# Optimization experiments

Measured on AMD Instinct MI355X. Metric: run time of the kernel, lower is better.

The kernel has to match this reference:

```python
import jax, jax.numpy as jnp
import numpy as np

B, C, H, W = 2, 64, 128, 128
K, SCALE, NUM_RES = 3, 2, 2
KK = K * K


def conv(x, w, b, pad=0):
    y = jax.lax.conv_general_dilated(x, w, (1, 1), [(pad, pad), (pad, pad)],
                                     dimension_numbers=('NCHW', 'OIHW', 'NCHW'))
    return y + b[None, :, None, None]


def unfold_dilated(x, k, d):
    # mimics nn.Unfold(kernel_size=k, dilation=d, padding=(k//2)*d) -> (b, c, k*k, h, w)
    pad = (k // 2) * d
    b, c, h, w = x.shape
    xp = jnp.pad(x, ((0, 0), (0, 0), (pad, pad), (pad, pad)))
    slices = [xp[:, :, i * d:i * d + h, j * d:j * d + w]
              for i in range(k) for j in range(k)]
    return jnp.stack(slices, axis=2)


def setup_inputs() -> dict:
    key = jax.random.key(0)
    ks = jax.random.split(key, 32)
    def p(k, shape, s=0.05):
        return jax.random.normal(k, shape, dtype=jnp.float32) * s
    H2, W2 = H * SCALE, W * SCALE
    return {
        'depth':  p(ks[0], (B, C, H2, W2), 1.0),
        'guide':  p(ks[1], (B, C, H2, W2), 1.0),
        'inputs': p(ks[2], (B, C, H, W), 1.0),
        # depth_kernel branch: 1x1 C->C (ReLU), 1x1 C->k^2
        'dk_w1': p(ks[3], (C, C, 1, 1)), 'dk_b1': jnp.zeros((C,), jnp.float32),
        'dk_w2': p(ks[4], (KK, C, 1, 1)), 'dk_b2': jnp.zeros((KK,), jnp.float32),
        # guide_kernel branch
        'gk_w1': p(ks[5], (C, C, 1, 1)), 'gk_b1': jnp.zeros((C,), jnp.float32),
        'gk_w2': p(ks[6], (KK, C, 1, 1)), 'gk_b2': jnp.zeros((KK,), jnp.float32),
        # weight_net: 3x3 2C->C (ReLU), 3x3 C->C (ReLU, TUnet stand-in), 3x3 C->1
        'wn_w1': p(ks[7], (C, 2 * C, 3, 3)), 'wn_b1': jnp.zeros((C,), jnp.float32),
        'wn_w2': p(ks[8], (C, C, 3, 3)), 'wn_b2': jnp.zeros((C,), jnp.float32),
        'wn_w3': p(ks[9], (1, C, 3, 3)), 'wn_b3': jnp.zeros((1,), jnp.float32),
        # residual blocks on inputs: NUM_RES x (conv3x3-ReLU-conv3x3 + skip)
        'rb_w': p(ks[10], (NUM_RES, 2, C, C, 3, 3)),
        'rb_b': jnp.zeros((NUM_RES, 2, C), jnp.float32),
        'aff_scale': 0.5 * KK * jnp.ones((1,), jnp.float32),
    }


def reference(depth, guide, inputs,
              dk_w1, dk_b1, dk_w2, dk_b2,
              gk_w1, gk_b1, gk_w2, gk_b2,
              wn_w1, wn_b1, wn_w2, wn_b2, wn_w3, wn_b3,
              rb_w, rb_b, aff_scale):
    # weight map
    wm = jax.nn.relu(conv(jnp.concatenate([depth, guide], axis=1), wn_w1, wn_b1, 1))
    wm = jax.nn.relu(conv(wm, wn_w2, wn_b2, 1))
    weight_map = conv(wm, wn_w3, wn_b3, 1)                       # (b,1,h_,w_)
    # per-pixel kernels
    dk = conv(jax.nn.relu(conv(depth, dk_w1, dk_b1)), dk_w2, dk_b2)
    gk = conv(jax.nn.relu(conv(guide, gk_w1, gk_b1)), gk_w2, gk_b2)
    dk = jax.nn.softmax(dk, axis=1)
    gk = jax.nn.softmax(gk, axis=1)
    fuse = weight_map * dk + (1.0 - weight_map) * gk
    fuse = jnp.tanh(fuse) / (aff_scale + 1e-8)
    ksum = jnp.maximum(jnp.sum(jnp.abs(fuse), axis=1, keepdims=True) + 1e-4, 1.0)
    fuse = fuse / ksum                                            # (b,k^2,h_,w_)
    # residual conv stack on low-res inputs
    x = inputs
    for i in range(NUM_RES):
        r = jax.nn.relu(conv(x, rb_w[i, 0], rb_b[i, 0], 1))
        r = conv(r, rb_w[i, 1], rb_b[i, 1], 1)
        x = x + r
    b, c, h, w = x.shape
    up = jax.image.resize(x, (b, c, h * SCALE, w * SCALE), method='bilinear')
    unf = unfold_dilated(up, K, SCALE)                            # (b,c,k^2,h_,w_)
    out = jnp.einsum('bkhw,bckhw->bchw', fuse, unf)
    return out
```

## Files before the change

### kernel.cpp

```cpp
#include <hip/hip_runtime.h>
#include <hip/hip_bf16.h>
#include <math.h>

#define HW2 (256*256)
#define HW1 (128*128)

typedef __attribute__((ext_vector_type(8))) short short8;
typedef __attribute__((ext_vector_type(4))) float floatx4;

__device__ __forceinline__ float b2f(ushort u) {
    union { unsigned int i; float f; } v; v.i = ((unsigned int)u) << 16; return v.f;
}
__device__ __forceinline__ ushort f2b(float f) {
    __hip_bfloat16 h = __float2bfloat16(f); return *(ushort*)&h;
}

__global__ __launch_bounds__(256)
void repack_w_bf16(const float* __restrict__ w, ushort* __restrict__ wt, int Cin) {
    int idx = blockIdx.x * 256 + threadIdx.x;
    int total = 64 * Cin * 9;
    if (idx >= total) return;
    int o   = idx / (Cin * 9);
    int rem = idx - o * (Cin * 9);
    int ci  = rem / 9;
    int t   = rem - ci * 9;
    int cc = ci >> 5, cl = ci & 31;
    wt[(((size_t)cc * 9 + t) * 64 + o) * 32 + cl] = f2b(w[idx]);
}

__global__ __launch_bounds__(256)
void repack_w64_batched(const float* __restrict__ wn_w2, const float* __restrict__ rb_w,
                        ushort* __restrict__ wt_wn2, ushort* __restrict__ wt_rb) {
    int idx = blockIdx.x * 256 + threadIdx.x;
    if (idx >= 36864) return;
    int set = blockIdx.y;
    const float* w = (set == 0) ? wn_w2 : rb_w + (size_t)(set - 1) * 36864;
    ushort* wt     = (set == 0) ? wt_wn2 : wt_rb + (size_t)(set - 1) * 36864;
    int o   = idx / 576;
    int rem = idx - o * 576;
    int ci  = rem / 9;
    int t   = rem - ci * 9;
    int cc = ci >> 5, cl = ci & 31;
    wt[(((size_t)cc * 9 + t) * 64 + o) * 32 + cl] = f2b(w[idx]);
}

__global__ __launch_bounds__(256)
void repack_1x1(const float* __restrict__ dk_w1, const float* __restrict__ gk_w1,
                const float* __restrict__ dk_w2, const float* __restrict__ gk_w2,
                ushort* __restrict__ w1d, ushort* __restrict__ w1g,
                ushort* __restrict__ w2d, ushort* __restrict__ w2g) {
    int idx = blockIdx.x * 256 + threadIdx.x;
    int set = blockIdx.y;
    if (set < 2) {
        if (idx >= 4096) return;
        const float* s = set == 0 ? dk_w1 : gk_w1;
        ushort* d = set == 0 ? w1d : w1g;
        d[idx] = f2b(s[idx]);
    } else {
        if (idx >= 1024) return;
        const float* s = set == 2 ? dk_w2 : gk_w2;
        ushort* d = set == 2 ? w2d : w2g;
        int row = idx >> 6;
        d[idx] = (row < 9) ? f2b(s[idx]) : (ushort)0;
    }
}

__global__ __launch_bounds__(256)
void to_chunked(const float* __restrict__ in, ushort* __restrict__ outc,
                int H, int W, int Cchunks) {
    int P = W + 2, Q = H + 2;
    int plane_px = P * Q;
    int idx = blockIdx.x * 256 + threadIdx.x;
    if (idx >= plane_px) return;
    int py = idx / P, px = idx - py * P;
    int bc = blockIdx.y;
    int b = bc / Cchunks, cc = bc - b * Cchunks;
    ushort* dst = outc + ((size_t)bc * plane_px + idx) * 32;
    if (py == 0 || py == Q - 1 || px == 0 || px == P - 1) {
        for (int c = 0; c < 32; ++c) dst[c] = 0;
        return;
    }
    int y = py - 1, x = px - 1;
    const float* src = in + ((size_t)b * (Cchunks * 32) + cc * 32) * H * W
                          + (size_t)y * W + x;
    for (int c = 0; c < 32; ++c)
        dst[c] = f2b(src[(size_t)c * H * W]);
}

__global__ __launch_bounds__(256)
void to_chunked_hi(const float* __restrict__ depth, const float* __restrict__ guide,
                   ushort* __restrict__ outc) {
    const int P = 258;
    int plane_px = P * P;
    int idx = blockIdx.x * 256 + threadIdx.x;
    if (idx >= plane_px) return;
    int py = idx / P, px = idx - py * P;
    int pl = blockIdx.y;
    const float* srcb = (pl < 4) ? depth : guide;
    int bc = pl & 3;
    int b = bc >> 1, cc = bc & 1;
    ushort* dst = outc + ((size_t)pl * plane_px + idx) * 32;
    if (py == 0 || py == P - 1 || px == 0 || px == P - 1) {
        for (int c = 0; c < 32; ++c) dst[c] = 0;
        return;
    }
    int y = py - 1, x = px - 1;
    const float* src = srcb + ((size_t)b * 64 + cc * 32) * HW2 + (size_t)y * 256 + x;
    for (int c = 0; c < 32; ++c)
        dst[c] = f2b(src[(size_t)c * HW2]);
}

__global__ __launch_bounds__(256)
void zero_border(ushort* __restrict__ buf, int H, int W, int nplanes) {
    int P = W + 2, Q = H + 2;
    int nb = 2 * P + 2 * H;
    int idx = blockIdx.x * 256 + threadIdx.x;
    if (idx >= nb * nplanes) return;
    int pl = idx / nb, r = idx - pl * nb;
    int py, px;
    if (r < P)          { py = 0;     px = r; }
    else if (r < 2 * P) { py = Q - 1; px = r - P; }
    else { int k = r - 2 * P; py = 1 + (k >> 1); px = (k & 1) ? P - 1 : 0; }
    ushort* dst = buf + ((size_t)pl * P * Q + (size_t)py * P + px) * 32;
    for (int c = 0; c < 32; ++c) dst[c] = 0;
}

template<int NCHUNK, bool RELU, bool HAS_SKIP, bool CONCAT2>
__global__ __launch_bounds__(256)
void conv3x3_reg(const ushort* __restrict__ inA, const ushort* __restrict__ inB,
                 const ushort* __restrict__ wt, const float* __restrict__ bias,
                 const ushort* __restrict__ skip, ushort* __restrict__ outc,
                 int H, int W) {
    const int P = W + 2;
    const size_t plane = (size_t)P * (H + 2) * 32;
    int tid = threadIdx.x;
    int wv = tid >> 6, lane = tid & 63, ml = lane & 15, q = lane >> 4;
    int x0 = blockIdx.x * 16;
    int rowsPerBlock = (blockDim.x >> 6) * 4;
    int yb = blockIdx.y * rowsPerBlock + wv * 4;
    int b = blockIdx.z;

    floatx4 acc[4][4];
#pragma unroll
    for (int r = 0; r < 4; ++r)
#pragma unroll
        for (int n = 0; n < 4; ++n) acc[r][n] = (floatx4){0.f, 0.f, 0.f, 0.f};

    for (int cc = 0; cc < NCHUNK; ++cc) {
        const ushort* base;
        if (CONCAT2) {
            constexpr int HC = NCHUNK / 2;
            if (cc < HC) base = inA + ((size_t)(b * HC + cc)) * plane;
            else         base = inB + ((size_t)(b * HC + cc - HC)) * plane;
        } else {
            base = inA + ((size_t)(b * NCHUNK + cc)) * plane;
        }
        const ushort* wb = wt + (size_t)cc * 18432;
#pragma unroll
        for (int t = 0; t < 9; ++t) {
            int dy = t / 3, dx = t - 3 * dy;
            short8 afr[4], bfr[4];
#pragma unroll
            for (int r = 0; r < 4; ++r)
                afr[r] = *(const short8*)&base[((size_t)(yb + r + dy) * P
                                               + (x0 + ml + dx)) * 32 + q * 8];
#pragma unroll
            for (int n = 0; n < 4; ++n)
                bfr[n] = *(const short8*)&wb[(size_t)(t * 64 + n * 16 + ml) * 32 + q * 8];
#pragma unroll
            for (int r = 0; r < 4; ++r)
#pragma unroll
                for (int n = 0; n < 4; ++n)
                    acc[r][n] = __builtin_amdgcn_mfma_f32_16x16x32_bf16(
                        afr[r], bfr[n], acc[r][n], 0, 0, 0);
        }
    }

#pragma unroll
    for (int r = 0; r < 4; ++r) {
        int y = yb + r;
#pragma unroll
        for (int n = 0; n < 4; ++n) {
            int ch = n * 16 + ml;
            int occ = ch >> 5, ocl = ch & 31;
            float bs = bias[ch];
            size_t pbase = ((size_t)(b * 2 + occ)) * plane + ((size_t)(y + 1) * P) * 32 + ocl;
#pragma unroll
            for (int e = 0; e < 4; ++e) {
                int x = x0 + q * 4 + e;
                float v = acc[r][n][e] + bs;
                if (RELU) v = fmaxf(v, 0.f);
                if (HAS_SKIP)
                    v += b2f(skip[((size_t)(b * 2 + occ)) * plane
                                  + ((size_t)(y + 1) * P + (x + 1)) * 32 + ocl]);
                outc[pbase + (size_t)(x + 1) * 32] = f2b(v);
            }
        }
    }
}

__global__ __launch_bounds__(256)
void conv3x3_1out_c(const ushort* __restrict__ inc, const float* __restrict__ w,
                    const float* __restrict__ bias, float* __restrict__ out) {
    __shared__ float wl[576];
    int tid = threadIdx.x;
    for (int i = tid; i < 576; i += 256) wl[i] = w[i];
    __syncthreads();

    int x = blockIdx.x * 16 + (tid & 15);
    int y = blockIdx.y * 16 + (tid >> 4);
    int b = blockIdx.z;
    const int P = 258;
    const size_t plane = (size_t)P * 258 * 32;

    float acc = bias[0];
    for (int cc = 0; cc < 2; ++cc) {
        const ushort* base = inc + ((size_t)(b * 2 + cc)) * plane;
#pragma unroll
        for (int t = 0; t < 9; ++t) {
            int dy = t / 3, dx = t - 3 * dy;
            const ushort* p = base + ((size_t)(y + dy) * P + (x + dx)) * 32;
            for (int c = 0; c < 32; ++c)
                acc = fmaf(wl[(cc * 32 + c) * 9 + t], b2f(p[c]), acc);
        }
    }
    out[(size_t)b * HW2 + y * 256 + x] = acc;
}

__global__ __launch_bounds__(256)
void kernels_fuse_mfma(const ushort* __restrict__ depth_c, const ushort* __restrict__ guide_c,
                       const float* __restrict__ wmap,
                       const ushort* __restrict__ w1d, const float* __restrict__ b1d,
                       const ushort* __restrict__ w2d, const float* __restrict__ b2d,
                       const ushort* __restrict__ w1g, const float* __restrict__ b1g,
                       const ushort* __restrict__ w2g, const float* __restrict__ b2g,
                       const float* __restrict__ aff, float* __restrict__ fuse_out) {
    __shared__ __align__(16) ushort hid[2][4][16 * 72];

    int tid = threadIdx.x;
    int wv = tid >> 6, lane = tid & 63, ml = lane & 15, q = lane >> 4;
    int p0 = blockIdx.x * 64 + wv * 16;
    int b = p0 >> 16, rem0 = p0 & 65535;
    const size_t plane = (size_t)258 * 258 * 32;

    int rem = rem0 + ml;
    int y = rem >> 8, x = rem & 255;
    size_t poff = ((size_t)(y + 1) * 258 + (x + 1)) * 32;

    float sm[2][4];

    for (int br = 0; br < 2; ++br) {
        const ushort* src = br ? guide_c : depth_c;
        const ushort* w1  = br ? w1g : w1d;
        const float*  b1  = br ? b1g : b1d;
        const ushort* w2  = br ? w2g : w2d;
        const float*  b2  = br ? b2g : b2d;
        ushort* h = hid[br][wv];

        short8 afr[2];
#pragma unroll
        for (int kc = 0; kc < 2; ++kc)
            afr[kc] = *(const short8*)&src[(size_t)(b * 2 + kc) * plane + poff + q * 8];

        floatx4 acc[4];
#pragma unroll
        for (int nt = 0; nt < 4; ++nt) acc[nt] = (floatx4){0.f, 0.f, 0.f, 0.f};
#pragma unroll
        for (int nt = 0; nt < 4; ++nt)
#pragma unroll
            for (int kc = 0; kc < 2; ++kc) {
                short8 bfr = *(const short8*)&w1[(size_t)((nt * 16 + ml) * 64 + kc * 32 + q * 8)];
                acc[nt] = __builtin_amdgcn_mfma_f32_16x16x32_bf16(afr[kc], bfr, acc[nt], 0, 0, 0);
            }

#pragma unroll
        for (int nt = 0; nt < 4; ++nt) {
            float bs = b1[nt * 16 + ml];
#pragma unroll
            for (int e = 0; e < 4; ++e) {
                float v = acc[nt][e] + bs;
                v = fmaxf(v, 0.f);
                h[(q * 4 + e) * 72 + nt * 16 + ml] = f2b(v);
            }
        }
        __syncthreads();

        floatx4 d2 = (floatx4){0.f, 0.f, 0.f, 0.f};
#pragma unroll
        for (int kc = 0; kc < 2; ++kc) {
            short8 a2 = *(const short8*)&w2[(size_t)(ml * 64 + kc * 32 + q * 8)];
            short8 hf = *(const short8*)&h[ml * 72 + kc * 32 + q * 8];
            d2 = __builtin_amdgcn_mfma_f32_16x16x32_bf16(a2, hf, d2, 0, 0, 0);
        }

        float lg[4];
#pragma unroll
        for (int e = 0; e < 4; ++e) {
            int j = q * 4 + e;
            lg[e] = (j < 9) ? (d2[e] + b2[j]) : -1e30f;
        }
        float m = fmaxf(fmaxf(lg[0], lg[1]), fmaxf(lg[2], lg[3]));
        m = fmaxf(m, __shfl_xor(m, 16));
        m = fmaxf(m, __shfl_xor(m, 32));
        float s = 0.f;
#pragma unroll
        for (int e = 0; e < 4; ++e) { lg[e] = __expf(lg[e] - m); s += lg[e]; }
        s += __shfl_xor(s, 16);
        s += __shfl_xor(s, 32);
        float inv = 1.f / s;
#pragma unroll
        for (int e = 0; e < 4; ++e) sm[br][e] = lg[e] * inv;
    }

    float wm = wmap[p0 + ml];
    float inv_av = 1.f / (aff[0] + 1e-8f);
    float f[4];
    float s = 0.f;
#pragma unroll
    for (int e = 0; e < 4; ++e) {
        float v = wm * sm[0][e] + (1.f - wm) * sm[1][e];
        v = tanhf(v) * inv_av;
        f[e] = v;
        s += fabsf(v);
    }
    s += __shfl_xor(s, 16);
    s += __shfl_xor(s, 32);
    float ksum = s + 1e-4f;
    if (ksum < 1.f) ksum = 1.f;
    float invk = 1.f / ksum;
#pragma unroll
    for (int e = 0; e < 4; ++e) {
        int j = q * 4 + e;
        if (j < 9)
            fuse_out[((size_t)b * 9 + j) * HW2 + rem0 + ml] = f[e] * invk;
    }
}

__global__ __launch_bounds__(256)
void upsample2x_c(const ushort* __restrict__ inc, ushort* __restrict__ outc) {
    int idx = blockIdx.x * 256 + threadIdx.x;
    if (idx >= 260 * 260) return;
    int py = idx / 260, px = idx - py * 260;
    int pl = blockIdx.y;
    ushort* dst = outc + ((size_t)pl * 260 * 260 + idx) * 32;
    if (py < 2 || py >= 258 || px < 2 || px >= 258) {
        for (int c = 0; c < 32; ++c) dst[c] = 0;
        return;
    }
    int y = py - 2, x = px - 2;

    int ylo, yhi; float wylo, wyhi;
    if (y & 1) { ylo = y >> 1; yhi = ylo + 1; if (yhi > 127) yhi = 127; wylo = 0.75f; wyhi = 0.25f; }
    else       { yhi = y >> 1; ylo = yhi - 1; if (ylo < 0)   ylo = 0;   wyhi = 0.75f; wylo = 0.25f; }
    int xlo, xhi; float wxlo, wxhi;
    if (x & 1) { xlo = x >> 1; xhi = xlo + 1; if (xhi > 127) xhi = 127; wxlo = 0.75f; wxhi = 0.25f; }
    else       { xhi = x >> 1; xlo = xhi - 1; if (xlo < 0)   xlo = 0;   wxhi = 0.75f; wxlo = 0.25f; }

    const ushort* base = inc + (size_t)pl * 130 * 130 * 32;
    const ushort* p00 = base + ((size_t)(ylo + 1) * 130 + (xlo + 1)) * 32;
    const ushort* p01 = base + ((size_t)(ylo + 1) * 130 + (xhi + 1)) * 32;
    const ushort* p10 = base + ((size_t)(yhi + 1) * 130 + (xlo + 1)) * 32;
    const ushort* p11 = base + ((size_t)(yhi + 1) * 130 + (xhi + 1)) * 32;
#pragma unroll
    for (int c = 0; c < 32; ++c) {
        float v = wylo * (wxlo * b2f(p00[c]) + wxhi * b2f(p01[c]))
                + wyhi * (wxlo * b2f(p10[c]) + wxhi * b2f(p11[c]));
        dst[c] = f2b(v);
    }
}

__global__ __launch_bounds__(256)
void fuse_apply_c(const float* __restrict__ fuse, const ushort* __restrict__ up,
                  float* __restrict__ out) {
    int p = blockIdx.x * 256 + threadIdx.x;
    int pl = blockIdx.y;
    int b = pl >> 1, cc = pl & 1;
    int y = p >> 8, x = p & 255;

    const float* f = fuse + (size_t)b * 9 * HW2 + p;
    const ushort* ub = up + (size_t)pl * 260 * 260 * 32;

    float acc[32];
#pragma unroll
    for (int c = 0; c < 32; ++c) acc[c] = 0.f;
#pragma unroll
    for (int t = 0; t < 9; ++t) {
        int dy = (t / 3 - 1) * 2, dx = (t % 3 - 1) * 2;
        float fv = f[(size_t)t * HW2];
        const ushort* u = ub + ((size_t)(y + 2 + dy) * 260 + (x + 2 + dx)) * 32;
#pragma unroll
        for (int c = 0; c < 32; ++c) acc[c] = fmaf(fv, b2f(u[c]), acc[c]);
    }
    float* ob = out + ((size_t)(b * 64 + cc * 32)) * HW2 + p;
#pragma unroll
    for (int c = 0; c < 32; ++c) ob[(size_t)c * HW2] = acc[c];
}

extern "C" void kernel_launch(void* const* d_in, const int* in_sizes, int n_in,
                              void* d_out, int out_size, void* d_ws, size_t ws_size,
                              hipStream_t stream) {
    const float* depth  = (const float*)d_in[0];
    const float* guide  = (const float*)d_in[1];
    const float* inputs = (const float*)d_in[2];
    const float* dk_w1  = (const float*)d_in[3];
    const float* dk_b1  = (const float*)d_in[4];
    const float* dk_w2  = (const float*)d_in[5];
    const float* dk_b2  = (const float*)d_in[6];
    const float* gk_w1  = (const float*)d_in[7];
    const float* gk_b1  = (const float*)d_in[8];
    const float* gk_w2  = (const float*)d_in[9];
    const float* gk_b2  = (const float*)d_in[10];
    const float* wn_w1  = (const float*)d_in[11];
    const float* wn_b1  = (const float*)d_in[12];
    const float* wn_w2  = (const float*)d_in[13];
    const float* wn_b2  = (const float*)d_in[14];
    const float* wn_w3  = (const float*)d_in[15];
    const float* wn_b3  = (const float*)d_in[16];
    const float* rb_w   = (const float*)d_in[17];
    const float* rb_b   = (const float*)d_in[18];
    const float* aff    = (const float*)d_in[19];
    float* out = (float*)d_out;

    float* ws = (float*)d_ws;
    size_t off = 0;
    const size_t CH256 = 4260096;
    const size_t CH128 = 1081600;
    ushort* depth_c = (ushort*)(ws + off); off += CH256;
    ushort* guide_c = (ushort*)(ws + off); off += CH256;
    ushort* bufA    = (ushort*)(ws + off); off += CH256;
    ushort* bufB    = (ushort*)(ws + off); off += CH256;
    ushort* up      = bufA;
    ushort* inp_c   = (ushort*)(ws + off); off += CH128;
    ushort* r0      = (ushort*)(ws + off); off += CH128;
    ushort* r1      = (ushort*)(ws + off); off += CH128;
    ushort* r2      = (ushort*)(ws + off); off += CH128;
    float* fuse     = ws + off; off += 1179648;
    float* wmap     = ws + off; off += 131072;
    ushort* wt_wn1  = (ushort*)(ws + off); off += 36864;
    ushort* wt_wn2  = (ushort*)(ws + off); off += 18432;
    ushort* wt_rb   = (ushort*)(ws + off); off += 73728;
    ushort* w1d_b   = (ushort*)(ws + off); off += 2048;
    ushort* w1g_b   = (ushort*)(ws + off); off += 2048;
    ushort* w2d_b   = (ushort*)(ws + off); off += 512;
    ushort* w2g_b   = (ushort*)(ws + off); off += 512;

    repack_w_bf16<<<288, 256, 0, stream>>>(wn_w1, wt_wn1, 128);
    repack_w64_batched<<<dim3(144, 5), 256, 0, stream>>>(wn_w2, rb_w, wt_wn2, wt_rb);
    repack_1x1<<<dim3(16, 4), 256, 0, stream>>>(dk_w1, gk_w1, dk_w2, gk_w2,
                                                w1d_b, w1g_b, w2d_b, w2g_b);

    to_chunked_hi<<<dim3(261, 8), 256, 0, stream>>>(depth, guide, depth_c);
    to_chunked<<<dim3(67, 4), 256, 0, stream>>>(inputs, inp_c, 128, 128, 2);

    zero_border<<<17, 256, 0, stream>>>(bufA, 256, 256, 8);
    zero_border<<<9,  256, 0, stream>>>(r0,   128, 128, 8);

    conv3x3_reg<4, true, false, true ><<<dim3(16, 16, 2), 256, 0, stream>>>(
        depth_c, guide_c, wt_wn1, wn_b1, nullptr, bufA, 256, 256);
    conv3x3_reg<2, true, false, false><<<dim3(16, 16, 2), 256, 0, stream>>>(
        bufA, nullptr, wt_wn2, wn_b2, nullptr, bufB, 256, 256);
    conv3x3_1out_c<<<dim3(16, 16, 2), 256, 0, stream>>>(bufB, wn_w3, wn_b3, wmap);

    kernels_fuse_mfma<<<2048, 256, 0, stream>>>(depth_c, guide_c, wmap,
                                                w1d_b, dk_b1, w2d_b, dk_b2,
                                                w1g_b, gk_b1, w2g_b, gk_b2,
                                                aff, fuse);

    conv3x3_reg<2, true,  false, false><<<dim3(8, 16, 2), 128, 0, stream>>>(
        inp_c, nullptr, wt_rb + 0 * 36864, rb_b + 0 * 64, nullptr, r0, 128, 128);
    conv3x3_reg<2, false, true,  false><<<dim3(8, 16, 2), 128, 0, stream>>>(
        r0, nullptr, wt_rb + 1 * 36864, rb_b + 1 * 64, inp_c, r1, 128, 128);
    conv3x3_reg<2, true,  false, false><<<dim3(8, 16, 2), 128, 0, stream>>>(
        r1, nullptr, wt_rb + 2 * 36864, rb_b + 2 * 64, nullptr, r0, 128, 128);
    conv3x3_reg<2, false, true,  false><<<dim3(8, 16, 2), 128, 0, stream>>>(
        r0, nullptr, wt_rb + 3 * 36864, rb_b + 3 * 64, r1, r2, 128, 128);

    upsample2x_c<<<dim3(265, 4), 256, 0, stream>>>(r2, up);
    fuse_apply_c<<<dim3(256, 4), 256, 0, stream>>>(fuse, up, out);
}
```

Measured before the change: 350.2 us.

## Fuse bilinear upsample into apply and weight-map conv into kernel-fuse

The separate bilinear upsample kernel is removed. The 3x3 dilated taps are now folded with the bilinear weights into a 4x4 coefficient grid, so the final apply kernel reads the low-res residual output directly instead of a materialized upsampled buffer. The single-output 3x3 weight-map conv moves into the per-pixel kernel-fusion kernel, which drops the wmap buffer. The three weight-repack launches are merged into one, the two border-zero launches are merged into one, and the residual convs now run 2 rows per wave with 256-thread blocks. This trades several launches and a large intermediate write and read for more gather loads and register pressure in the fused kernels.

```diff
diff --git a/kernel.cpp b/kernel.cpp
--- a/kernel.cpp
+++ b/kernel.cpp
@@ -16,52 +16,34 @@
 }
 
 __global__ __launch_bounds__(256)
-void repack_w_bf16(const float* __restrict__ w, ushort* __restrict__ wt, int Cin) {
-    int idx = blockIdx.x * 256 + threadIdx.x;
-    int total = 64 * Cin * 9;
-    if (idx >= total) return;
-    int o   = idx / (Cin * 9);
-    int rem = idx - o * (Cin * 9);
-    int ci  = rem / 9;
-    int t   = rem - ci * 9;
-    int cc = ci >> 5, cl = ci & 31;
-    wt[(((size_t)cc * 9 + t) * 64 + o) * 32 + cl] = f2b(w[idx]);
-}
-
-__global__ __launch_bounds__(256)
-void repack_w64_batched(const float* __restrict__ wn_w2, const float* __restrict__ rb_w,
-                        ushort* __restrict__ wt_wn2, ushort* __restrict__ wt_rb) {
-    int idx = blockIdx.x * 256 + threadIdx.x;
-    if (idx >= 36864) return;
-    int set = blockIdx.y;
-    const float* w = (set == 0) ? wn_w2 : rb_w + (size_t)(set - 1) * 36864;
-    ushort* wt     = (set == 0) ? wt_wn2 : wt_rb + (size_t)(set - 1) * 36864;
-    int o   = idx / 576;
-    int rem = idx - o * 576;
-    int ci  = rem / 9;
-    int t   = rem - ci * 9;
-    int cc = ci >> 5, cl = ci & 31;
-    wt[(((size_t)cc * 9 + t) * 64 + o) * 32 + cl] = f2b(w[idx]);
-}
-
-__global__ __launch_bounds__(256)
-void repack_1x1(const float* __restrict__ dk_w1, const float* __restrict__ gk_w1,
+void repack_all(const float* __restrict__ wn_w1, const float* __restrict__ wn_w2,
+                const float* __restrict__ rb_w,
+                const float* __restrict__ dk_w1, const float* __restrict__ gk_w1,
                 const float* __restrict__ dk_w2, const float* __restrict__ gk_w2,
+                ushort* __restrict__ wt_wn1, ushort* __restrict__ wt_wn2,
+                ushort* __restrict__ wt_rb,
                 ushort* __restrict__ w1d, ushort* __restrict__ w1g,
                 ushort* __restrict__ w2d, ushort* __restrict__ w2g) {
     int idx = blockIdx.x * 256 + threadIdx.x;
-    int set = blockIdx.y;
-    if (set < 2) {
-        if (idx >= 4096) return;
-        const float* s = set == 0 ? dk_w1 : gk_w1;
-        ushort* d = set == 0 ? w1d : w1g;
-        d[idx] = f2b(s[idx]);
+    int role = blockIdx.y;
+    if (role == 0) {
+        if (idx >= 73728) return;
+        int o = idx / 1152; int rem = idx - o * 1152;
+        int ci = rem / 9;   int t = rem - ci * 9;
+        wt_wn1[(((size_t)(ci >> 5) * 9 + t) * 64 + o) * 32 + (ci & 31)] = f2b(wn_w1[idx]);
+    } else if (role <= 5) {
+        if (idx >= 36864) return;
+        const float* w = (role == 1) ? wn_w2 : rb_w + (size_t)(role - 2) * 36864;
+        ushort* wt     = (role == 1) ? wt_wn2 : wt_rb + (size_t)(role - 2) * 36864;
+        int o = idx / 576; int rem = idx - o * 576;
+        int ci = rem / 9;  int t = rem - ci * 9;
+        wt[(((size_t)(ci >> 5) * 9 + t) * 64 + o) * 32 + (ci & 31)] = f2b(w[idx]);
     } else {
-        if (idx >= 1024) return;
-        const float* s = set == 2 ? dk_w2 : gk_w2;
-        ushort* d = set == 2 ? w2d : w2g;
-        int row = idx >> 6;
-        d[idx] = (row < 9) ? f2b(s[idx]) : (ushort)0;
+        if (idx >= 10240) return;
+        if (idx < 4096)      w1d[idx] = f2b(dk_w1[idx]);
+        else if (idx < 8192) w1g[idx - 4096] = f2b(gk_w1[idx - 4096]);
+        else if (idx < 9216) { int i = idx - 8192; w2d[i] = (i >> 6) < 9 ? f2b(dk_w2[i]) : (ushort)0; }
+        else                 { int i = idx - 9216; w2g[i] = (i >> 6) < 9 ? f2b(gk_w2[i]) : (ushort)0; }
     }
 }
 
@@ -111,11 +93,14 @@
 }
 
 __global__ __launch_bounds__(256)
-void zero_border(ushort* __restrict__ buf, int H, int W, int nplanes) {
-    int P = W + 2, Q = H + 2;
+void zero_border2(ushort* __restrict__ buf256, ushort* __restrict__ buf128) {
+    int region = blockIdx.y;
+    int H = region ? 128 : 256;
+    int P = H + 2, Q = H + 2;
+    ushort* buf = region ? buf128 : buf256;
     int nb = 2 * P + 2 * H;
     int idx = blockIdx.x * 256 + threadIdx.x;
-    if (idx >= nb * nplanes) return;
+    if (idx >= nb * 8) return;
     int pl = idx / nb, r = idx - pl * nb;
     int py, px;
     if (r < P)          { py = 0;     px = r; }
@@ -125,7 +110,7 @@
     for (int c = 0; c < 32; ++c) dst[c] = 0;
 }
 
-template<int NCHUNK, bool RELU, bool HAS_SKIP, bool CONCAT2>
+template<int NCHUNK, int ROWS, bool RELU, bool HAS_SKIP, bool CONCAT2>
 __global__ __launch_bounds__(256)
 void conv3x3_reg(const ushort* __restrict__ inA, const ushort* __restrict__ inB,
                  const ushort* __restrict__ wt, const float* __restrict__ bias,
@@ -136,13 +121,13 @@
     int tid = threadIdx.x;
     int wv = tid >> 6, lane = tid & 63, ml = lane & 15, q = lane >> 4;
     int x0 = blockIdx.x * 16;
-    int rowsPerBlock = (blockDim.x >> 6) * 4;
-    int yb = blockIdx.y * rowsPerBlock + wv * 4;
+    int rowsPerBlock = (blockDim.x >> 6) * ROWS;
+    int yb = blockIdx.y * rowsPerBlock + wv * ROWS;
     int b = blockIdx.z;
 
-    floatx4 acc[4][4];
-#pragma unroll
-    for (int r = 0; r < 4; ++r)
+    floatx4 acc[ROWS][4];
+#pragma unroll
+    for (int r = 0; r < ROWS; ++r)
 #pragma unroll
         for (int n = 0; n < 4; ++n) acc[r][n] = (floatx4){0.f, 0.f, 0.f, 0.f};
 
@@ -159,16 +144,16 @@
 #pragma unroll
         for (int t = 0; t < 9; ++t) {
             int dy = t / 3, dx = t - 3 * dy;
-            short8 afr[4], bfr[4];
-#pragma unroll
-            for (int r = 0; r < 4; ++r)
+            short8 afr[ROWS], bfr[4];
+#pragma unroll
+            for (int r = 0; r < ROWS; ++r)
                 afr[r] = *(const short8*)&base[((size_t)(yb + r + dy) * P
                                                + (x0 + ml + dx)) * 32 + q * 8];
 #pragma unroll
             for (int n = 0; n < 4; ++n)
                 bfr[n] = *(const short8*)&wb[(size_t)(t * 64 + n * 16 + ml) * 32 + q * 8];
 #pragma unroll
-            for (int r = 0; r < 4; ++r)
+            for (int r = 0; r < ROWS; ++r)
 #pragma unroll
                 for (int n = 0; n < 4; ++n)
                     acc[r][n] = __builtin_amdgcn_mfma_f32_16x16x32_bf16(
@@ -177,7 +162,7 @@
     }
 
 #pragma unroll
-    for (int r = 0; r < 4; ++r) {
+    for (int r = 0; r < ROWS; ++r) {
         int y = yb + r;
 #pragma unroll
         for (int n = 0; n < 4; ++n) {
@@ -200,44 +185,21 @@
 }
 
 __global__ __launch_bounds__(256)
-void conv3x3_1out_c(const ushort* __restrict__ inc, const float* __restrict__ w,
-                    const float* __restrict__ bias, float* __restrict__ out) {
-    __shared__ float wl[576];
-    int tid = threadIdx.x;
-    for (int i = tid; i < 576; i += 256) wl[i] = w[i];
-    __syncthreads();
-
-    int x = blockIdx.x * 16 + (tid & 15);
-    int y = blockIdx.y * 16 + (tid >> 4);
-    int b = blockIdx.z;
-    const int P = 258;
-    const size_t plane = (size_t)P * 258 * 32;
-
-    float acc = bias[0];
-    for (int cc = 0; cc < 2; ++cc) {
-        const ushort* base = inc + ((size_t)(b * 2 + cc)) * plane;
-#pragma unroll
-        for (int t = 0; t < 9; ++t) {
-            int dy = t / 3, dx = t - 3 * dy;
-            const ushort* p = base + ((size_t)(y + dy) * P + (x + dx)) * 32;
-            for (int c = 0; c < 32; ++c)
-                acc = fmaf(wl[(cc * 32 + c) * 9 + t], b2f(p[c]), acc);
-        }
-    }
-    out[(size_t)b * HW2 + y * 256 + x] = acc;
-}
-
-__global__ __launch_bounds__(256)
 void kernels_fuse_mfma(const ushort* __restrict__ depth_c, const ushort* __restrict__ guide_c,
-                       const float* __restrict__ wmap,
+                       const ushort* __restrict__ bufB,
+                       const float* __restrict__ wn_w3, const float* __restrict__ wn_b3,
                        const ushort* __restrict__ w1d, const float* __restrict__ b1d,
                        const ushort* __restrict__ w2d, const float* __restrict__ b2d,
                        const ushort* __restrict__ w1g, const float* __restrict__ b1g,
                        const ushort* __restrict__ w2g, const float* __restrict__ b2g,
                        const float* __restrict__ aff, float* __restrict__ fuse_out) {
     __shared__ __align__(16) ushort hid[2][4][16 * 72];
+    __shared__ float wl[576];
 
     int tid = threadIdx.x;
+    for (int i = tid; i < 576; i += 256) wl[i] = wn_w3[i];
+    __syncthreads();
+
     int wv = tid >> 6, lane = tid & 63, ml = lane & 15, q = lane >> 4;
     int p0 = blockIdx.x * 64 + wv * 16;
     int b = p0 >> 16, rem0 = p0 & 65535;
@@ -247,8 +209,19 @@
     int y = rem >> 8, x = rem & 255;
     size_t poff = ((size_t)(y + 1) * 258 + (x + 1)) * 32;
 
+    float wm = wn_b3[0];
+    for (int cc = 0; cc < 2; ++cc) {
+        const ushort* basep = bufB + (size_t)(b * 2 + cc) * plane;
+#pragma unroll
+        for (int t = 0; t < 9; ++t) {
+            int dy = t / 3, dx = t - 3 * dy;
+            const ushort* pp = basep + ((size_t)(y + dy) * 258 + (x + dx)) * 32;
+            for (int c = 0; c < 32; ++c)
+                wm = fmaf(wl[(cc * 32 + c) * 9 + t], b2f(pp[c]), wm);
+        }
+    }
+
     float sm[2][4];
-
     for (int br = 0; br < 2; ++br) {
         const ushort* src = br ? guide_c : depth_c;
         const ushort* w1  = br ? w1g : w1d;
@@ -283,7 +256,6 @@
                 h[(q * 4 + e) * 72 + nt * 16 + ml] = f2b(v);
             }
         }
-        __syncthreads();
 
         floatx4 d2 = (floatx4){0.f, 0.f, 0.f, 0.f};
 #pragma unroll
@@ -312,7 +284,6 @@
         for (int e = 0; e < 4; ++e) sm[br][e] = lg[e] * inv;
     }
 
-    float wm = wmap[p0 + ml];
     float inv_av = 1.f / (aff[0] + 1e-8f);
     float f[4];
     float s = 0.f;
@@ -337,59 +308,57 @@
 }
 
 __global__ __launch_bounds__(256)
-void upsample2x_c(const ushort* __restrict__ inc, ushort* __restrict__ outc) {
-    int idx = blockIdx.x * 256 + threadIdx.x;
-    if (idx >= 260 * 260) return;
-    int py = idx / 260, px = idx - py * 260;
-    int pl = blockIdx.y;
-    ushort* dst = outc + ((size_t)pl * 260 * 260 + idx) * 32;
-    if (py < 2 || py >= 258 || px < 2 || px >= 258) {
-        for (int c = 0; c < 32; ++c) dst[c] = 0;
-        return;
-    }
-    int y = py - 2, x = px - 2;
-
-    int ylo, yhi; float wylo, wyhi;
-    if (y & 1) { ylo = y >> 1; yhi = ylo + 1; if (yhi > 127) yhi = 127; wylo = 0.75f; wyhi = 0.25f; }
-    else       { yhi = y >> 1; ylo = yhi - 1; if (ylo < 0)   ylo = 0;   wyhi = 0.75f; wylo = 0.25f; }
-    int xlo, xhi; float wxlo, wxhi;
-    if (x & 1) { xlo = x >> 1; xhi = xlo + 1; if (xhi > 127) xhi = 127; wxlo = 0.75f; wxhi = 0.25f; }
-    else       { xhi = x >> 1; xlo = xhi - 1; if (xlo < 0)   xlo = 0;   wxhi = 0.75f; wxlo = 0.25f; }
-
-    const ushort* base = inc + (size_t)pl * 130 * 130 * 32;
-    const ushort* p00 = base + ((size_t)(ylo + 1) * 130 + (xlo + 1)) * 32;
-    const ushort* p01 = base + ((size_t)(ylo + 1) * 130 + (xhi + 1)) * 32;
-    const ushort* p10 = base + ((size_t)(yhi + 1) * 130 + (xlo + 1)) * 32;
-    const ushort* p11 = base + ((size_t)(yhi + 1) * 130 + (xhi + 1)) * 32;
-#pragma unroll
-    for (int c = 0; c < 32; ++c) {
-        float v = wylo * (wxlo * b2f(p00[c]) + wxhi * b2f(p01[c]))
-                + wyhi * (wxlo * b2f(p10[c]) + wxhi * b2f(p11[c]));
-        dst[c] = f2b(v);
-    }
-}
-
-__global__ __launch_bounds__(256)
-void fuse_apply_c(const float* __restrict__ fuse, const ushort* __restrict__ up,
-                  float* __restrict__ out) {
+void fuse_apply_up(const float* __restrict__ fuse, const ushort* __restrict__ r2c,
+                   float* __restrict__ out) {
     int p = blockIdx.x * 256 + threadIdx.x;
     int pl = blockIdx.y;
     int b = pl >> 1, cc = pl & 1;
     int y = p >> 8, x = p & 255;
 
+    int my = y >> 1, mx = x >> 1;
+    float wyA = (y & 1) ? 0.75f : 0.25f;  float wyB = 1.f - wyA;
+    float wxA = (x & 1) ? 0.75f : 0.25f;  float wxB = 1.f - wxA;
+    int R0y = my + ((y & 1) ? 0 : -1) - 1;
+    int R0x = mx + ((x & 1) ? 0 : -1) - 1;
+
     const float* f = fuse + (size_t)b * 9 * HW2 + p;
-    const ushort* ub = up + (size_t)pl * 260 * 260 * 32;
-
+    float coef[4][4];
+#pragma unroll
+    for (int k = 0; k < 4; ++k)
+#pragma unroll
+        for (int l = 0; l < 4; ++l) coef[k][l] = 0.f;
+
+#pragma unroll
+    for (int ty = 0; ty < 3; ++ty) {
+        int yp = y + (ty - 1) * 2;
+        if (yp < 0 || yp > 255) continue;
+#pragma unroll
+        for (int tx = 0; tx < 3; ++tx) {
+            int xp = x + (tx - 1) * 2;
+            if (xp < 0 || xp > 255) continue;
+            float fv = f[(size_t)(ty * 3 + tx) * HW2];
+            coef[ty][tx]         += fv * wyA * wxA;
+            coef[ty][tx + 1]     += fv * wyA * wxB;
+            coef[ty + 1][tx]     += fv * wyB * wxA;
+            coef[ty + 1][tx + 1] += fv * wyB * wxB;
+        }
+    }
+
+    const ushort* base = r2c + (size_t)pl * 130 * 130 * 32;
     float acc[32];
 #pragma unroll
     for (int c = 0; c < 32; ++c) acc[c] = 0.f;
 #pragma unroll
-    for (int t = 0; t < 9; ++t) {
-        int dy = (t / 3 - 1) * 2, dx = (t % 3 - 1) * 2;
-        float fv = f[(size_t)t * HW2];
-        const ushort* u = ub + ((size_t)(y + 2 + dy) * 260 + (x + 2 + dx)) * 32;
-#pragma unroll
-        for (int c = 0; c < 32; ++c) acc[c] = fmaf(fv, b2f(u[c]), acc[c]);
+    for (int k = 0; k < 4; ++k) {
+        int ry = R0y + k; ry = ry < 0 ? 0 : (ry > 127 ? 127 : ry);
+#pragma unroll
+        for (int l = 0; l < 4; ++l) {
+            int rx = R0x + l; rx = rx < 0 ? 0 : (rx > 127 ? 127 : rx);
+            float cf = coef[k][l];
+            const ushort* u = base + ((size_t)(ry + 1) * 130 + (rx + 1)) * 32;
+#pragma unroll
+            for (int c = 0; c < 32; ++c) acc[c] = fmaf(cf, b2f(u[c]), acc[c]);
+        }
     }
     float* ob = out + ((size_t)(b * 64 + cc * 32)) * HW2 + p;
 #pragma unroll
@@ -429,13 +398,11 @@
     ushort* guide_c = (ushort*)(ws + off); off += CH256;
     ushort* bufA    = (ushort*)(ws + off); off += CH256;
     ushort* bufB    = (ushort*)(ws + off); off += CH256;
-    ushort* up      = bufA;
     ushort* inp_c   = (ushort*)(ws + off); off += CH128;
     ushort* r0      = (ushort*)(ws + off); off += CH128;
     ushort* r1      = (ushort*)(ws + off); off += CH128;
     ushort* r2      = (ushort*)(ws + off); off += CH128;
     float* fuse     = ws + off; off += 1179648;
-    float* wmap     = ws + off; off += 131072;
     ushort* wt_wn1  = (ushort*)(ws + off); off += 36864;
     ushort* wt_wn2  = (ushort*)(ws + off); off += 18432;
     ushort* wt_rb   = (ushort*)(ws + off); off += 73728;
@@ -444,37 +411,34 @@
     ushort* w2d_b   = (ushort*)(ws + off); off += 512;
     ushort* w2g_b   = (ushort*)(ws + off); off += 512;
 
-    repack_w_bf16<<<288, 256, 0, stream>>>(wn_w1, wt_wn1, 128);
-    repack_w64_batched<<<dim3(144, 5), 256, 0, stream>>>(wn_w2, rb_w, wt_wn2, wt_rb);
-    repack_1x1<<<dim3(16, 4), 256, 0, stream>>>(dk_w1, gk_w1, dk_w2, gk_w2,
-                                                w1d_b, w1g_b, w2d_b, w2g_b);
+    repack_all<<<dim3(288, 7), 256, 0, stream>>>(
+        wn_w1, wn_w2, rb_w, dk_w1, gk_w1, dk_w2, gk_w2,
+        wt_wn1, wt_wn2, wt_rb, w1d_b, w1g_b, w2d_b, w2g_b);
 
     to_chunked_hi<<<dim3(261, 8), 256, 0, stream>>>(depth, guide, depth_c);
     to_chunked<<<dim3(67, 4), 256, 0, stream>>>(inputs, inp_c, 128, 128, 2);
 
-    zero_border<<<17, 256, 0, stream>>>(bufA, 256, 256, 8);
-    zero_border<<<9,  256, 0, stream>>>(r0,   128, 128, 8);
-
-    conv3x3_reg<4, true, false, true ><<<dim3(16, 16, 2), 256, 0, stream>>>(
+    zero_border2<<<dim3(33, 2), 256, 0, stream>>>(bufA, r0);
+
+    conv3x3_reg<4, 4, true, false, true ><<<dim3(16, 16, 2), 256, 0, stream>>>(
         depth_c, guide_c, wt_wn1, wn_b1, nullptr, bufA, 256, 256);
-    conv3x3_reg<2, true, false, false><<<dim3(16, 16, 2), 256, 0, stream>>>(
+    conv3x3_reg<2, 4, true, false, false><<<dim3(16, 16, 2), 256, 0, stream>>>(
         bufA, nullptr, wt_wn2, wn_b2, nullptr, bufB, 256, 256);
-    conv3x3_1out_c<<<dim3(16, 16, 2), 256, 0, stream>>>(bufB, wn_w3, wn_b3, wmap);
-
-    kernels_fuse_mfma<<<2048, 256, 0, stream>>>(depth_c, guide_c, wmap,
+
+    kernels_fuse_mfma<<<2048, 256, 0, stream>>>(depth_c, guide_c, bufB,
+                                                wn_w3, wn_b3,
                                                 w1d_b, dk_b1, w2d_b, dk_b2,
                                                 w1g_b, gk_b1, w2g_b, gk_b2,
                                                 aff, fuse);
 
-    conv3x3_reg<2, true,  false, false><<<dim3(8, 16, 2), 128, 0, stream>>>(
+    conv3x3_reg<2, 2, true,  false, false><<<dim3(8, 16, 2), 256, 0, stream>>>(
         inp_c, nullptr, wt_rb + 0 * 36864, rb_b + 0 * 64, nullptr, r0, 128, 128);
-    conv3x3_reg<2, false, true,  false><<<dim3(8, 16, 2), 128, 0, stream>>>(
+    conv3x3_reg<2, 2, false, true,  false><<<dim3(8, 16, 2), 256, 0, stream>>>(
         r0, nullptr, wt_rb + 1 * 36864, rb_b + 1 * 64, inp_c, r1, 128, 128);
-    conv3x3_reg<2, true,  false, false><<<dim3(8, 16, 2), 128, 0, stream>>>(
+    conv3x3_reg<2, 2, true,  false, false><<<dim3(8, 16, 2), 256, 0, stream>>>(
         r1, nullptr, wt_rb + 2 * 36864, rb_b + 2 * 64, nullptr, r0, 128, 128);
-    conv3x3_reg<2, false, true,  false><<<dim3(8, 16, 2), 128, 0, stream>>>(
+    conv3x3_reg<2, 2, false, true,  false><<<dim3(8, 16, 2), 256, 0, stream>>>(
         r0, nullptr, wt_rb + 3 * 36864, rb_b + 3 * 64, r1, r2, 128, 128);
 
-    upsample2x_c<<<dim3(265, 4), 256, 0, stream>>>(r2, up);
-    fuse_apply_c<<<dim3(256, 4), 256, 0, stream>>>(fuse, up, out);
-}
+    fuse_apply_up<<<dim3(256, 4), 256, 0, stream>>>(fuse, r2, out);
+}
```

Measured after the change: 368.6 us. 5.3% more time.
